# Performance work log

Measured on AMD Instinct MI355X. Metric: run time of the kernel, lower is better.

Reference implementation:

```python
import jax, jax.numpy as jnp
import numpy as np

D_CHAR, D_HID, LEN_VOC = 256, 1024, 512
BSZ, MAX_LEN = 128, 256


def setup_inputs() -> dict:
    key = jax.random.key(0)
    ks = jax.random.split(key, 14)
    s = 1.0 / np.sqrt(D_HID)  # PyTorch RNN/Linear init scale
    u = lambda k, shape: jax.random.uniform(k, shape, jnp.float32, -s, s)
    return {
        "inputs": jax.random.randint(ks[0], (BSZ, MAX_LEN), 0, LEN_VOC),
        "outputs": jax.random.randint(ks[1], (BSZ, MAX_LEN), 0, LEN_VOC),
        "emb": jax.random.normal(ks[2], (LEN_VOC, D_CHAR), jnp.float32),
        "enc_Wih": u(ks[3], (D_HID, D_CHAR)),
        "enc_Whh": u(ks[4], (D_HID, D_HID)),
        "enc_bih": u(ks[5], (D_HID,)),
        "enc_bhh": u(ks[6], (D_HID,)),
        "dec_Wih": u(ks[7], (D_HID, D_CHAR)),
        "dec_Whh": u(ks[8], (D_HID, D_HID)),
        "dec_bih": u(ks[9], (D_HID,)),
        "dec_bhh": u(ks[10], (D_HID,)),
        "out_W": u(ks[11], (LEN_VOC, D_HID)),
        "out_b": u(ks[12], (LEN_VOC,)),
    }


def rnn_scan(x_seq, h0, Wih, Whh, bih, bhh):
    """Elman RNN (tanh), batch_first input [B, T, D] -> (h_T [B,H], all h [T,B,H]).
    h_t = tanh(W_ih x_t + b_ih + W_hh h_{t-1} + b_hh), matching torch.nn.RNN."""
    # Precompute input projection for all timesteps (one big GEMM).
    xp = jnp.einsum('btd,hd->bth', x_seq, Wih) + bih + bhh  # [B,T,H]
    xp = jnp.swapaxes(xp, 0, 1)  # [T,B,H] for scan

    def step(h, x):
        h = jnp.tanh(x + h @ Whh.T)
        return h, h

    hT, hs = jax.lax.scan(step, h0, xp)
    return hT, hs


def reference(inputs, outputs, emb, enc_Wih, enc_Whh, enc_bih, enc_bhh,
              dec_Wih, dec_Whh, dec_bih, dec_bhh, out_W, out_b):
    bsz, max_len = inputs.shape
    # Encoder over input char embeddings, zero initial hidden.
    embs = emb[inputs]  # [B,T,Dc]
    h0 = jnp.zeros((bsz, D_HID), jnp.float32)
    hT, _ = rnn_scan(embs, h0, enc_Wih, enc_Whh, enc_bih, enc_bhh)
    # Teacher-forced decoder: step 0 gets zero input, step t gets emb(outputs[:, t-1]).
    dec_in = jnp.concatenate(
        [jnp.zeros((bsz, 1, D_CHAR), jnp.float32), emb[outputs[:, :-1]]], axis=1)
    _, dec_hs = rnn_scan(dec_in, hT, dec_Wih, dec_Whh, dec_bih, dec_bhh)  # [T,B,H]
    # decoder_states.transpose(0,1).view(-1, d_hid)
    states = jnp.swapaxes(dec_hs, 0, 1).reshape(-1, D_HID)  # [B*T, H]
    logits = states @ out_W.T + out_b  # [B*T, V]
    return jax.nn.log_softmax(logits, axis=1)
```

## Files before the change

kernel.cpp:

```cpp
#include <hip/hip_runtime.h>


typedef short short8 __attribute__((ext_vector_type(8)));
typedef float floatx4 __attribute__((ext_vector_type(4)));

#define WS_XP_ENC  0ull
#define WS_XP_DEC  (64ull << 20)
#define WS_STATES  (128ull << 20)
#define WS_H       (192ull << 20)
#define WS_FLAGS   ((192ull << 20) + (512ull << 10))
#define WS_WB5     (193ull << 20)
#define WS_HENC    (192ull << 20)
#define WS_FLAGS2  (256ull << 20)
#define WS_WB6     ((256ull << 20) + (1ull << 20))
#define FAST_NEED  ((265ull) << 20)

#define HS_STRIDE 1032

__device__ __forceinline__ float bf2f(unsigned short u) {
  union { unsigned u; float f; } x; x.u = ((unsigned)u) << 16; return x.f;
}
__device__ __forceinline__ unsigned short f2bf(float f) {
  union { float f; unsigned u; } x; x.f = f;
  unsigned r = x.u + 0x7FFFu + ((x.u >> 16) & 1u);
  return (unsigned short)(r >> 16);
}
__device__ __forceinline__ unsigned pkminu16(unsigned a, unsigned b) {
  unsigned d;
  asm("v_pk_min_u16 %0, %1, %2" : "=v"(d) : "v"(a), "v"(b));
  return d;
}

__global__ __launch_bounds__(256) void cvt_kernel(
    const float* __restrict__ src, unsigned short* __restrict__ dst, int n)
{
  const int i = (blockIdx.x * 256 + threadIdx.x) * 4;
  if (i >= n) return;
  const float4 v = *(const float4*)(src + i);
  unsigned short o[4] = {f2bf(v.x), f2bf(v.y), f2bf(v.z), f2bf(v.w)};
  *(uint2*)(dst + i) = *(const uint2*)o;
}

__global__ __launch_bounds__(256) void gemm_bt_kernel(
    const unsigned short* __restrict__ Abase,
    const int* __restrict__ gidx, const int mode,
    const unsigned short* __restrict__ Bmat,
    const float* __restrict__ bias0,
    const float* __restrict__ bias1,
    unsigned short* __restrict__ outp_bf,
    float* __restrict__ outp_f,
    const int K, const int N, const int nbn)
{
  __shared__ unsigned short As[64][264];
  __shared__ unsigned short Bs[64][264];
  __shared__ const unsigned short* rowsrc[64];

  const int tid = threadIdx.x;
  const int lane = tid & 63;
  const int wave = tid >> 6;
  const int bn = blockIdx.x % nbn;
  const int bm = blockIdx.x / nbn;
  const int m0 = bm * 64;
  const int j0 = bn * 64;

  if (tid < 64) {
    const int m = m0 + tid;
    const unsigned short* src;
    if (mode == 0) {
      src = Abase + (size_t)m * K;
    } else if (mode == 3) {
      src = Abase + ((size_t)(m & 255) * 128 + (m >> 8)) * 1024;
    } else {
      const int t = m >> 7;
      const int b = m & 127;
      if (mode == 2 && t == 0) {
        src = nullptr;
      } else {
        const int v = (mode == 1) ? gidx[b * 256 + t] : gidx[b * 256 + t - 1];
        src = Abase + (size_t)v * 256;
      }
    }
    rowsrc[tid] = src;
  }

  const floatx4 zf = {0.f, 0.f, 0.f, 0.f};
  floatx4 acc0 = zf, acc1 = zf, acc2 = zf, acc3 = zf;

  for (int kc = 0; kc < K; kc += 256) {
    __syncthreads();
#pragma unroll
    for (int i = 0; i < 8; ++i) {
      const int idx = i * 256 + tid;
      const int r = idx >> 5;
      const int c = idx & 31;
      const unsigned short* s = rowsrc[r];
      short8 av = {0, 0, 0, 0, 0, 0, 0, 0};
      if (s) av = *(const short8*)(s + kc + c * 8);
      *(short8*)&As[r][c * 8] = av;
      *(short8*)&Bs[r][c * 8] =
          *(const short8*)(Bmat + (size_t)(j0 + r) * K + kc + c * 8);
    }
    __syncthreads();
    const int ar = 16 * wave + (lane & 15);
    const int kq = (lane >> 4) * 8;
#pragma unroll
    for (int kk = 0; kk < 8; ++kk) {
      const short8 a = *(const short8*)&As[ar][kk * 32 + kq];
      const short8 bv0 = *(const short8*)&Bs[(lane & 15)][kk * 32 + kq];
      acc0 = __builtin_amdgcn_mfma_f32_16x16x32_bf16(a, bv0, acc0, 0, 0, 0);
      const short8 bv1 = *(const short8*)&Bs[16 + (lane & 15)][kk * 32 + kq];
      acc1 = __builtin_amdgcn_mfma_f32_16x16x32_bf16(a, bv1, acc1, 0, 0, 0);
      const short8 bv2 = *(const short8*)&Bs[32 + (lane & 15)][kk * 32 + kq];
      acc2 = __builtin_amdgcn_mfma_f32_16x16x32_bf16(a, bv2, acc2, 0, 0, 0);
      const short8 bv3 = *(const short8*)&Bs[48 + (lane & 15)][kk * 32 + kq];
      acc3 = __builtin_amdgcn_mfma_f32_16x16x32_bf16(a, bv3, acc3, 0, 0, 0);
    }
  }

  float bs[4] = {0.f, 0.f, 0.f, 0.f};
  if (bias0) {
#pragma unroll
    for (int nt = 0; nt < 4; ++nt) {
      const int jj = j0 + nt * 16 + (lane & 15);
      bs[nt] = bias0[jj] + bias1[jj];
    }
  }
  __syncthreads();
  const int rbase = 16 * wave + (lane >> 4) * 4;
  const int cl = lane & 15;

  if (outp_bf) {
#pragma unroll
    for (int i = 0; i < 4; ++i) {
      As[rbase + i][cl]      = f2bf(acc0[i] + bs[0]);
      As[rbase + i][16 + cl] = f2bf(acc1[i] + bs[1]);
      As[rbase + i][32 + cl] = f2bf(acc2[i] + bs[2]);
      As[rbase + i][48 + cl] = f2bf(acc3[i] + bs[3]);
    }
    __syncthreads();
#pragma unroll
    for (int i = 0; i < 2; ++i) {
      const int idx = i * 256 + tid;
      const int r = idx >> 3;
      const int c = idx & 7;
      *(short8*)(outp_bf + (size_t)(m0 + r) * N + j0 + c * 8) =
          *(const short8*)&As[r][c * 8];
    }
  } else {
    float (*Asf)[66] = (float(*)[66]) & As[0][0];
#pragma unroll
    for (int i = 0; i < 4; ++i) {
      Asf[rbase + i][cl]      = acc0[i] + bs[0];
      Asf[rbase + i][16 + cl] = acc1[i] + bs[1];
      Asf[rbase + i][32 + cl] = acc2[i] + bs[2];
      Asf[rbase + i][48 + cl] = acc3[i] + bs[3];
    }
    __syncthreads();
#pragma unroll
    for (int i = 0; i < 4; ++i) {
      const int idx = i * 256 + tid;
      const int r = idx >> 4;
      const int c = idx & 15;
      *(float4*)(outp_f + (size_t)(m0 + r) * N + j0 + c * 4) =
          *(const float4*)&Asf[r][c * 4];
    }
  }
}

__global__ __launch_bounds__(256) void rnn_scan2_kernel(
    const unsigned short* __restrict__ WhhE,
    const unsigned short* __restrict__ WhhD,
    const unsigned short* __restrict__ xpE,
    const unsigned short* __restrict__ xpD,
    unsigned short* __restrict__ henc,
    unsigned short* __restrict__ hdec,
    unsigned int* __restrict__ flags)
{
  __shared__ unsigned short hs[16 * HS_STRIDE];
  __shared__ unsigned int okw[4];

  const int tid = threadIdx.x;
  const int lane = tid & 63;
  const int wave = tid >> 6;
  const int g = blockIdx.x & 7;
  const int slot = blockIdx.x >> 3;
  const int b0 = g * 16;
  const int q = lane >> 4;
  const int cl = lane & 15;
  const int j = slot * 64 + wave * 16 + cl;
  unsigned int* grpflags = flags + g * 32;

  short8 w[32];
  const floatx4 zf = {0.f, 0.f, 0.f, 0.f};

  for (int phase = 0; phase < 2; ++phase) {
    const unsigned short* Whh = phase ? WhhD : WhhE;
    const unsigned short* xp = phase ? xpD : xpE;
    {
      const unsigned short* wp = Whh + (size_t)j * 1024 + q * 8;
#pragma unroll
      for (int kk = 0; kk < 32; ++kk) w[kk] = *(const short8*)(wp + kk * 32);
    }
    for (int t = 0; t < 256; ++t) {
      const int s = phase * 256 + t;
      float xpv[4];
      const unsigned short* xprow = xp + (size_t)t * 131072;
#pragma unroll
      for (int i = 0; i < 4; ++i)
        xpv[i] = bf2f(xprow[(size_t)(b0 + q * 4 + i) * 1024 + j]);

      short8 tmp[8];
      const unsigned short* hprev =
          (s <= 256 ? henc + (size_t)(s - 1) * 131072
                    : hdec + (size_t)(s - 257) * 131072) + b0 * 1024;
      if (s > 0) {
#pragma unroll
        for (int c = 0; c < 8; ++c) {
          const int gg = c * 256 + tid;
          tmp[c] = *(const short8*)(hprev + gg * 8);
        }
        const unsigned* du = (const unsigned*)tmp;
        unsigned m0v = 0xFFFFFFFFu, m1v = 0xFFFFFFFFu;
        unsigned m2v = 0xFFFFFFFFu, m3v = 0xFFFFFFFFu;
#pragma unroll
        for (int i = 0; i < 8; ++i) {
          m0v = pkminu16(m0v, du[4 * i + 0] ^ 0xAAAAAAAAu);
          m1v = pkminu16(m1v, du[4 * i + 1] ^ 0xAAAAAAAAu);
          m2v = pkminu16(m2v, du[4 * i + 2] ^ 0xAAAAAAAAu);
          m3v = pkminu16(m3v, du[4 * i + 3] ^ 0xAAAAAAAAu);
        }
        const unsigned mm = pkminu16(pkminu16(m0v, m1v), pkminu16(m2v, m3v));
        const unsigned hz = (mm - 0x00010001u) & ~mm & 0x80008000u;
        const unsigned long long bad = __ballot(hz != 0u);
        if (lane == 0) okw[wave] = (bad != 0ull) ? 1u : 0u;
      } else {
        if (lane == 0) okw[wave] = 0u;
      }
      __syncthreads();
      const bool need_fb = (okw[0] | okw[1] | okw[2] | okw[3]) != 0u;
      if (s > 0 && need_fb) {
        if (wave == 0) {
          const unsigned target = (unsigned)s;
          for (;;) {
            const unsigned f = __hip_atomic_load(&grpflags[lane & 15],
                                                 __ATOMIC_RELAXED,
                                                 __HIP_MEMORY_SCOPE_AGENT);
            if (__ballot(f < target) == 0ull) break;
            __builtin_amdgcn_s_sleep(1);
          }
        }
        __syncthreads();
#pragma unroll
        for (int c = 0; c < 8; ++c) {
          const int gg = c * 256 + tid;
          const unsigned long long* p =
              (const unsigned long long*)(hprev + gg * 8);
          union { unsigned long long u[2]; short8 s8; } v;
          v.u[0] = __hip_atomic_load(p, __ATOMIC_RELAXED,
                                     __HIP_MEMORY_SCOPE_AGENT);
          v.u[1] = __hip_atomic_load(p + 1, __ATOMIC_RELAXED,
                                     __HIP_MEMORY_SCOPE_AGENT);
          tmp[c] = v.s8;
        }
      }
      if (s > 0) {
#pragma unroll
        for (int c = 0; c < 8; ++c) {
          const int gg = c * 256 + tid;
          *(short8*)&hs[(gg >> 7) * HS_STRIDE + (gg & 127) * 8] = tmp[c];
        }
      }
      __syncthreads();

      floatx4 acc0 = zf, acc1 = zf, acc2 = zf, acc3 = zf;
      if (s > 0) {
        const unsigned short* hrow = &hs[cl * HS_STRIDE + q * 8];
#pragma unroll
        for (int kk = 0; kk < 32; kk += 4) {
          const short8 a0 = *(const short8*)(hrow + (kk + 0) * 32);
          const short8 a1 = *(const short8*)(hrow + (kk + 1) * 32);
          const short8 a2 = *(const short8*)(hrow + (kk + 2) * 32);
          const short8 a3 = *(const short8*)(hrow + (kk + 3) * 32);
          acc0 = __builtin_amdgcn_mfma_f32_16x16x32_bf16(a0, w[kk], acc0, 0, 0, 0);
          acc1 = __builtin_amdgcn_mfma_f32_16x16x32_bf16(a1, w[kk + 1], acc1, 0, 0, 0);
          acc2 = __builtin_amdgcn_mfma_f32_16x16x32_bf16(a2, w[kk + 2], acc2, 0, 0, 0);
          acc3 = __builtin_amdgcn_mfma_f32_16x16x32_bf16(a3, w[kk + 3], acc3, 0, 0, 0);
        }
      }
      unsigned short* hw =
          phase ? hdec + (size_t)t * 131072 : henc + (size_t)s * 131072;
#pragma unroll
      for (int i = 0; i < 4; ++i) {
        const int br = b0 + q * 4 + i;
        const float pre = acc0[i] + acc1[i] + acc2[i] + acc3[i] + xpv[i];
        const float e = __expf(2.f * pre);
        const float hv = 1.f - 2.f / (e + 1.f);
        const unsigned short hb = f2bf(hv);
        __hip_atomic_store(&hw[(size_t)br * 1024 + j], hb, __ATOMIC_RELAXED,
                           __HIP_MEMORY_SCOPE_AGENT);
      }
      __syncthreads();
      if (tid == 0)
        __hip_atomic_store(&grpflags[slot], (unsigned)(s + 1), __ATOMIC_RELAXED,
                           __HIP_MEMORY_SCOPE_AGENT);
    }
  }
}

__global__ __launch_bounds__(256) void rnn_scan_kernel(
    const unsigned short* __restrict__ WhhE,
    const unsigned short* __restrict__ WhhD,
    const unsigned short* __restrict__ xpE,
    const unsigned short* __restrict__ xpD,
    unsigned short* __restrict__ hbuf,
    unsigned short* __restrict__ states,
    unsigned int* __restrict__ flags)
{
  __shared__ unsigned short hs[16 * HS_STRIDE];

  const int tid = threadIdx.x;
  const int lane = tid & 63;
  const int wave = tid >> 6;
  const int g = blockIdx.x & 7;
  const int slot = blockIdx.x >> 3;
  const int b0 = g * 16;
  const int q = lane >> 4;
  const int cl = lane & 15;
  const int j = slot * 64 + wave * 16 + cl;
  unsigned int* grpflags = flags + g * 32;

  short8 w[32];
  const floatx4 zf = {0.f, 0.f, 0.f, 0.f};

  for (int phase = 0; phase < 2; ++phase) {
    const unsigned short* Whh = phase ? WhhD : WhhE;
    const unsigned short* xp = phase ? xpD : xpE;
    {
      const unsigned short* wp = Whh + (size_t)j * 1024 + q * 8;
#pragma unroll
      for (int kk = 0; kk < 32; ++kk) w[kk] = *(const short8*)(wp + kk * 32);
    }
    for (int t = 0; t < 256; ++t) {
      const int s = phase * 256 + t;
      float xpv[4];
      const unsigned short* xprow = xp + (size_t)t * 131072;
#pragma unroll
      for (int i = 0; i < 4; ++i)
        xpv[i] = bf2f(xprow[(size_t)(b0 + q * 4 + i) * 1024 + j]);

      if (s > 0) {
        const unsigned short* hrb = hbuf + (size_t)(s & 1) * 131072 + b0 * 1024;
        unsigned long long tmp[16];
#pragma unroll
        for (int c = 0; c < 8; ++c) {
          const int gg = c * 256 + tid;
          const unsigned long long* p = (const unsigned long long*)(hrb + gg * 8);
          tmp[2 * c]     = __hip_atomic_load(p, __ATOMIC_RELAXED,
                                             __HIP_MEMORY_SCOPE_AGENT);
          tmp[2 * c + 1] = __hip_atomic_load(p + 1, __ATOMIC_RELAXED,
                                             __HIP_MEMORY_SCOPE_AGENT);
        }
#pragma unroll
        for (int c = 0; c < 8; ++c) {
          const int gg = c * 256 + tid;
          unsigned long long* d =
              (unsigned long long*)&hs[(gg >> 7) * HS_STRIDE + (gg & 127) * 8];
          d[0] = tmp[2 * c];
          d[1] = tmp[2 * c + 1];
        }
      }
      __syncthreads();

      floatx4 acc0 = zf, acc1 = zf, acc2 = zf, acc3 = zf;
      if (s > 0) {
        const unsigned short* hrow = &hs[cl * HS_STRIDE + q * 8];
#pragma unroll
        for (int kk = 0; kk < 32; kk += 4) {
          const short8 a0 = *(const short8*)(hrow + (kk + 0) * 32);
          const short8 a1 = *(const short8*)(hrow + (kk + 1) * 32);
          const short8 a2 = *(const short8*)(hrow + (kk + 2) * 32);
          const short8 a3 = *(const short8*)(hrow + (kk + 3) * 32);
          acc0 = __builtin_amdgcn_mfma_f32_16x16x32_bf16(a0, w[kk], acc0, 0, 0, 0);
          acc1 = __builtin_amdgcn_mfma_f32_16x16x32_bf16(a1, w[kk + 1], acc1, 0, 0, 0);
          acc2 = __builtin_amdgcn_mfma_f32_16x16x32_bf16(a2, w[kk + 2], acc2, 0, 0, 0);
          acc3 = __builtin_amdgcn_mfma_f32_16x16x32_bf16(a3, w[kk + 3], acc3, 0, 0, 0);
        }
      }
      unsigned short* hw = hbuf + (size_t)((s + 1) & 1) * 131072;
#pragma unroll
      for (int i = 0; i < 4; ++i) {
        const int br = b0 + q * 4 + i;
        const float pre = acc0[i] + acc1[i] + acc2[i] + acc3[i] + xpv[i];
        const float e = __expf(2.f * pre);
        const float hv = 1.f - 2.f / (e + 1.f);
        const unsigned short hb = f2bf(hv);
        __hip_atomic_store(&hw[(size_t)br * 1024 + j], hb, __ATOMIC_RELAXED,
                           __HIP_MEMORY_SCOPE_AGENT);
        if (phase) states[((size_t)br * 256 + t) * 1024 + j] = hb;
      }
      __syncthreads();
      if (tid == 0)
        __hip_atomic_store(&grpflags[slot], (unsigned)(s + 1), __ATOMIC_RELAXED,
                           __HIP_MEMORY_SCOPE_AGENT);
      if (wave == 0) {
        const unsigned target = (unsigned)(s + 1);
        while (true) {
          const unsigned f = __hip_atomic_load(&grpflags[lane & 15],
                                               __ATOMIC_RELAXED,
                                               __HIP_MEMORY_SCOPE_AGENT);
          if (__ballot(f < target) == 0ull) break;
          __builtin_amdgcn_s_sleep(2);
        }
      }
      __syncthreads();
    }
  }
}

__global__ __launch_bounds__(256) void logsoftmax_kernel(
    float* __restrict__ logits, const float* __restrict__ outb)
{
  const int row = blockIdx.x * 4 + (threadIdx.x >> 6);
  const int lane = threadIdx.x & 63;
  float* rp = logits + (size_t)row * 512 + lane * 8;
  const float4 a0 = *(const float4*)rp;
  const float4 a1 = *(const float4*)(rp + 4);
  const float4 b0 = *(const float4*)(outb + lane * 8);
  const float4 b1 = *(const float4*)(outb + lane * 8 + 4);
  float v[8] = {a0.x + b0.x, a0.y + b0.y, a0.z + b0.z, a0.w + b0.w,
                a1.x + b1.x, a1.y + b1.y, a1.z + b1.z, a1.w + b1.w};
  float mx = v[0];
#pragma unroll
  for (int i = 1; i < 8; ++i) mx = fmaxf(mx, v[i]);
#pragma unroll
  for (int m = 1; m < 64; m <<= 1) mx = fmaxf(mx, __shfl_xor(mx, m, 64));
  float sum = 0.f;
#pragma unroll
  for (int i = 0; i < 8; ++i) sum += __expf(v[i] - mx);
#pragma unroll
  for (int m = 1; m < 64; m <<= 1) sum += __shfl_xor(sum, m, 64);
  const float lse = mx + __logf(sum);
  float4 o0 = {v[0] - lse, v[1] - lse, v[2] - lse, v[3] - lse};
  float4 o1 = {v[4] - lse, v[5] - lse, v[6] - lse, v[7] - lse};
  *(float4*)rp = o0;
  *(float4*)(rp + 4) = o1;
}

extern "C" void kernel_launch(void* const* d_in, const int* in_sizes, int n_in,
                              void* d_out, int out_size, void* d_ws, size_t ws_size,
                              hipStream_t stream)
{
  const int* inputs  = (const int*)d_in[0];
  const int* outputs = (const int*)d_in[1];
  const float* emb    = (const float*)d_in[2];
  const float* encWih = (const float*)d_in[3];
  const float* encWhh = (const float*)d_in[4];
  const float* encBih = (const float*)d_in[5];
  const float* encBhh = (const float*)d_in[6];
  const float* decWih = (const float*)d_in[7];
  const float* decWhh = (const float*)d_in[8];
  const float* decBih = (const float*)d_in[9];
  const float* decBhh = (const float*)d_in[10];
  const float* outW   = (const float*)d_in[11];
  const float* outB   = (const float*)d_in[12];

  char* ws = (char*)d_ws;
  unsigned short* xpE    = (unsigned short*)(ws + WS_XP_ENC);
  unsigned short* xpD    = (unsigned short*)(ws + WS_XP_DEC);
  unsigned short* states = (unsigned short*)(ws + WS_STATES);
  float* logits = (float*)d_out;

  const bool fast = (ws_size >= (size_t)FAST_NEED);
  char* wb = ws + (fast ? WS_WB6 : WS_WB5);
  unsigned short* embB  = (unsigned short*)(wb + 0);
  unsigned short* eWihB = (unsigned short*)(wb + (512ull << 10));
  unsigned short* dWihB = (unsigned short*)(wb + (1ull << 20));
  unsigned short* eWhhB = (unsigned short*)(wb + (2ull << 20));
  unsigned short* dWhhB = (unsigned short*)(wb + (4ull << 20));
  unsigned short* outWB = (unsigned short*)(wb + (6ull << 20));

  cvt_kernel<<<128, 256, 0, stream>>>(emb, embB, 512 * 256);
  cvt_kernel<<<256, 256, 0, stream>>>(encWih, eWihB, 1024 * 256);
  cvt_kernel<<<256, 256, 0, stream>>>(decWih, dWihB, 1024 * 256);
  cvt_kernel<<<1024, 256, 0, stream>>>(encWhh, eWhhB, 1024 * 1024);
  cvt_kernel<<<1024, 256, 0, stream>>>(decWhh, dWhhB, 1024 * 1024);
  cvt_kernel<<<512, 256, 0, stream>>>(outW, outWB, 512 * 1024);

  gemm_bt_kernel<<<8192, 256, 0, stream>>>(embB, inputs, 1, eWihB, encBih, encBhh,
                                           xpE, nullptr, 256, 1024, 16);
  gemm_bt_kernel<<<8192, 256, 0, stream>>>(embB, outputs, 2, dWihB, decBih, decBhh,
                                           xpD, nullptr, 256, 1024, 16);

  if (fast) {
    unsigned short* henc = (unsigned short*)(ws + WS_HENC);
    unsigned short* hdec = states;
    unsigned int* flags2 = (unsigned int*)(ws + WS_FLAGS2);
    hipMemsetAsync(flags2, 0, 4096, stream);
    rnn_scan2_kernel<<<128, 256, 0, stream>>>(eWhhB, dWhhB, xpE, xpD,
                                              henc, hdec, flags2);
    gemm_bt_kernel<<<4096, 256, 0, stream>>>(hdec, nullptr, 3, outWB, nullptr,
                                             nullptr, nullptr, logits, 1024, 512, 8);
  } else {
    unsigned short* hbuf = (unsigned short*)(ws + WS_H);
    unsigned int* flags = (unsigned int*)(ws + WS_FLAGS);
    hipMemsetAsync(flags, 0, 4096, stream);
    rnn_scan_kernel<<<128, 256, 0, stream>>>(eWhhB, dWhhB, xpE, xpD, hbuf,
                                             states, flags);
    gemm_bt_kernel<<<4096, 256, 0, stream>>>(states, nullptr, 0, outWB, nullptr,
                                             nullptr, nullptr, logits, 1024, 512, 8);
  }
  logsoftmax_kernel<<<8192, 256, 0, stream>>>(logits, outB);
}
```

Before: 1.726 ms.

## Project vocabulary once and gather input projections by token inside scan

```diff
diff --git a/kernel.cpp b/kernel.cpp
--- a/kernel.cpp
+++ b/kernel.cpp
@@ -4,16 +4,9 @@
 typedef short short8 __attribute__((ext_vector_type(8)));
 typedef float floatx4 __attribute__((ext_vector_type(4)));
 
-#define WS_XP_ENC  0ull
-#define WS_XP_DEC  (64ull << 20)
-#define WS_STATES  (128ull << 20)
-#define WS_H       (192ull << 20)
-#define WS_FLAGS   ((192ull << 20) + (512ull << 10))
-#define WS_WB5     (193ull << 20)
-#define WS_HENC    (192ull << 20)
-#define WS_FLAGS2  (256ull << 20)
-#define WS_WB6     ((256ull << 20) + (1ull << 20))
-#define FAST_NEED  ((265ull) << 20)
+#define WS_HENC   0ull
+#define WS_HDEC   (64ull << 20)
+#define WS_WB     (128ull << 20)
 
 #define HS_STRIDE 1032
 
@@ -43,7 +36,7 @@
 
 __global__ __launch_bounds__(256) void gemm_bt_kernel(
     const unsigned short* __restrict__ Abase,
-    const int* __restrict__ gidx, const int mode,
+    const int mode,
     const unsigned short* __restrict__ Bmat,
     const float* __restrict__ bias0,
     const float* __restrict__ bias1,
@@ -68,17 +61,8 @@
     const unsigned short* src;
     if (mode == 0) {
       src = Abase + (size_t)m * K;
-    } else if (mode == 3) {
+    } else {
       src = Abase + ((size_t)(m & 255) * 128 + (m >> 8)) * 1024;
-    } else {
-      const int t = m >> 7;
-      const int b = m & 127;
-      if (mode == 2 && t == 0) {
-        src = nullptr;
-      } else {
-        const int v = (mode == 1) ? gidx[b * 256 + t] : gidx[b * 256 + t - 1];
-        src = Abase + (size_t)v * 256;
-      }
     }
     rowsrc[tid] = src;
   }
@@ -94,9 +78,7 @@
       const int r = idx >> 5;
       const int c = idx & 31;
       const unsigned short* s = rowsrc[r];
-      short8 av = {0, 0, 0, 0, 0, 0, 0, 0};
-      if (s) av = *(const short8*)(s + kc + c * 8);
-      *(short8*)&As[r][c * 8] = av;
+      *(short8*)&As[r][c * 8] = *(const short8*)(s + kc + c * 8);
       *(short8*)&Bs[r][c * 8] =
           *(const short8*)(Bmat + (size_t)(j0 + r) * K + kc + c * 8);
     }
@@ -167,16 +149,21 @@
   }
 }
 
-__global__ __launch_bounds__(256) void rnn_scan2_kernel(
+__global__ __launch_bounds__(256) void rnn_scan3_kernel(
     const unsigned short* __restrict__ WhhE,
     const unsigned short* __restrict__ WhhD,
-    const unsigned short* __restrict__ xpE,
-    const unsigned short* __restrict__ xpD,
+    const unsigned short* __restrict__ projE,
+    const unsigned short* __restrict__ projD,
+    const float* __restrict__ decBih,
+    const float* __restrict__ decBhh,
+    const int* __restrict__ intoks,
+    const int* __restrict__ outtoks,
     unsigned short* __restrict__ henc,
     unsigned short* __restrict__ hdec,
     unsigned int* __restrict__ flags)
 {
   __shared__ unsigned short hs[16 * HS_STRIDE];
+  __shared__ int toks[16 * 257];
   __shared__ unsigned int okw[4];
 
   const int tid = threadIdx.x;
@@ -187,7 +174,8 @@
   const int b0 = g * 16;
   const int q = lane >> 4;
   const int cl = lane & 15;
-  const int j = slot * 64 + wave * 16 + cl;
+  const int jwb = slot * 64 + wave * 16;
+  const int jq4 = jwb + q * 4;
   unsigned int* grpflags = flags + g * 32;
 
   short8 w[32];
@@ -195,19 +183,42 @@
 
   for (int phase = 0; phase < 2; ++phase) {
     const unsigned short* Whh = phase ? WhhD : WhhE;
-    const unsigned short* xp = phase ? xpD : xpE;
+    const unsigned short* proj = phase ? projD : projE;
+    const int* gt = phase ? outtoks : intoks;
     {
-      const unsigned short* wp = Whh + (size_t)j * 1024 + q * 8;
+      const unsigned short* wp = Whh + (size_t)(jwb + cl) * 1024 + q * 8;
 #pragma unroll
       for (int kk = 0; kk < 32; ++kk) w[kk] = *(const short8*)(wp + kk * 32);
     }
+    float xb[4] = {0.f, 0.f, 0.f, 0.f};
+    if (phase) {
+#pragma unroll
+      for (int i = 0; i < 4; ++i) xb[i] = decBih[jq4 + i] + decBhh[jq4 + i];
+    }
+    __syncthreads();
+#pragma unroll
+    for (int i = 0; i < 16; ++i) {
+      const int idx = i * 256 + tid;
+      toks[(idx >> 8) * 257 + (idx & 255)] =
+          gt[(size_t)(b0 + (idx >> 8)) * 256 + (idx & 255)];
+    }
+    __syncthreads();
+
     for (int t = 0; t < 256; ++t) {
       const int s = phase * 256 + t;
-      float xpv[4];
-      const unsigned short* xprow = xp + (size_t)t * 131072;
-#pragma unroll
-      for (int i = 0; i < 4; ++i)
-        xpv[i] = bf2f(xprow[(size_t)(b0 + q * 4 + i) * 1024 + j]);
+      float xpf[4];
+      {
+        const int tt = phase ? (t > 0 ? t - 1 : 0) : t;
+        const int tok = toks[cl * 257 + tt];
+        const uint2 xr = *(const uint2*)(proj + (size_t)tok * 1024 + jq4);
+        const unsigned short* xs = (const unsigned short*)&xr;
+#pragma unroll
+        for (int i = 0; i < 4; ++i) xpf[i] = bf2f(xs[i]);
+        if (phase && t == 0) {
+#pragma unroll
+          for (int i = 0; i < 4; ++i) xpf[i] = xb[i];
+        }
+      }
 
       short8 tmp[8];
       const unsigned short* hprev =
@@ -215,10 +226,8 @@
                     : hdec + (size_t)(s - 257) * 131072) + b0 * 1024;
       if (s > 0) {
 #pragma unroll
-        for (int c = 0; c < 8; ++c) {
-          const int gg = c * 256 + tid;
-          tmp[c] = *(const short8*)(hprev + gg * 8);
-        }
+        for (int c = 0; c < 8; ++c)
+          tmp[c] = *(const short8*)(hprev + (c * 256 + tid) * 8);
         const unsigned* du = (const unsigned*)tmp;
         unsigned m0v = 0xFFFFFFFFu, m1v = 0xFFFFFFFFu;
         unsigned m2v = 0xFFFFFFFFu, m3v = 0xFFFFFFFFu;
@@ -252,9 +261,8 @@
         __syncthreads();
 #pragma unroll
         for (int c = 0; c < 8; ++c) {
-          const int gg = c * 256 + tid;
           const unsigned long long* p =
-              (const unsigned long long*)(hprev + gg * 8);
+              (const unsigned long long*)(hprev + (c * 256 + tid) * 8);
           union { unsigned long long u[2]; short8 s8; } v;
           v.u[0] = __hip_atomic_load(p, __ATOMIC_RELAXED,
                                      __HIP_MEMORY_SCOPE_AGENT);
@@ -281,138 +289,29 @@
           const short8 a1 = *(const short8*)(hrow + (kk + 1) * 32);
           const short8 a2 = *(const short8*)(hrow + (kk + 2) * 32);
           const short8 a3 = *(const short8*)(hrow + (kk + 3) * 32);
-          acc0 = __builtin_amdgcn_mfma_f32_16x16x32_bf16(a0, w[kk], acc0, 0, 0, 0);
-          acc1 = __builtin_amdgcn_mfma_f32_16x16x32_bf16(a1, w[kk + 1], acc1, 0, 0, 0);
-          acc2 = __builtin_amdgcn_mfma_f32_16x16x32_bf16(a2, w[kk + 2], acc2, 0, 0, 0);
-          acc3 = __builtin_amdgcn_mfma_f32_16x16x32_bf16(a3, w[kk + 3], acc3, 0, 0, 0);
+          acc0 = __builtin_amdgcn_mfma_f32_16x16x32_bf16(w[kk + 0], a0, acc0, 0, 0, 0);
+          acc1 = __builtin_amdgcn_mfma_f32_16x16x32_bf16(w[kk + 1], a1, acc1, 0, 0, 0);
+          acc2 = __builtin_amdgcn_mfma_f32_16x16x32_bf16(w[kk + 2], a2, acc2, 0, 0, 0);
+          acc3 = __builtin_amdgcn_mfma_f32_16x16x32_bf16(w[kk + 3], a3, acc3, 0, 0, 0);
         }
       }
       unsigned short* hw =
           phase ? hdec + (size_t)t * 131072 : henc + (size_t)s * 131072;
+      unsigned short ob[4];
 #pragma unroll
       for (int i = 0; i < 4; ++i) {
-        const int br = b0 + q * 4 + i;
-        const float pre = acc0[i] + acc1[i] + acc2[i] + acc3[i] + xpv[i];
+        const float pre = acc0[i] + acc1[i] + acc2[i] + acc3[i] + xpf[i];
         const float e = __expf(2.f * pre);
-        const float hv = 1.f - 2.f / (e + 1.f);
-        const unsigned short hb = f2bf(hv);
-        __hip_atomic_store(&hw[(size_t)br * 1024 + j], hb, __ATOMIC_RELAXED,
-                           __HIP_MEMORY_SCOPE_AGENT);
-      }
+        ob[i] = f2bf(1.f - 2.f / (e + 1.f));
+      }
+      __hip_atomic_store(
+          (unsigned long long*)(hw + (size_t)(b0 + cl) * 1024 + jq4),
+          *(const unsigned long long*)ob, __ATOMIC_RELAXED,
+          __HIP_MEMORY_SCOPE_AGENT);
       __syncthreads();
       if (tid == 0)
         __hip_atomic_store(&grpflags[slot], (unsigned)(s + 1), __ATOMIC_RELAXED,
                            __HIP_MEMORY_SCOPE_AGENT);
-    }
-  }
-}
-
-__global__ __launch_bounds__(256) void rnn_scan_kernel(
-    const unsigned short* __restrict__ WhhE,
-    const unsigned short* __restrict__ WhhD,
-    const unsigned short* __restrict__ xpE,
-    const unsigned short* __restrict__ xpD,
-    unsigned short* __restrict__ hbuf,
-    unsigned short* __restrict__ states,
-    unsigned int* __restrict__ flags)
-{
-  __shared__ unsigned short hs[16 * HS_STRIDE];
-
-  const int tid = threadIdx.x;
-  const int lane = tid & 63;
-  const int wave = tid >> 6;
-  const int g = blockIdx.x & 7;
-  const int slot = blockIdx.x >> 3;
-  const int b0 = g * 16;
-  const int q = lane >> 4;
-  const int cl = lane & 15;
-  const int j = slot * 64 + wave * 16 + cl;
-  unsigned int* grpflags = flags + g * 32;
-
-  short8 w[32];
-  const floatx4 zf = {0.f, 0.f, 0.f, 0.f};
-
-  for (int phase = 0; phase < 2; ++phase) {
-    const unsigned short* Whh = phase ? WhhD : WhhE;
-    const unsigned short* xp = phase ? xpD : xpE;
-    {
-      const unsigned short* wp = Whh + (size_t)j * 1024 + q * 8;
-#pragma unroll
-      for (int kk = 0; kk < 32; ++kk) w[kk] = *(const short8*)(wp + kk * 32);
-    }
-    for (int t = 0; t < 256; ++t) {
-      const int s = phase * 256 + t;
-      float xpv[4];
-      const unsigned short* xprow = xp + (size_t)t * 131072;
-#pragma unroll
-      for (int i = 0; i < 4; ++i)
-        xpv[i] = bf2f(xprow[(size_t)(b0 + q * 4 + i) * 1024 + j]);
-
-      if (s > 0) {
-        const unsigned short* hrb = hbuf + (size_t)(s & 1) * 131072 + b0 * 1024;
-        unsigned long long tmp[16];
-#pragma unroll
-        for (int c = 0; c < 8; ++c) {
-          const int gg = c * 256 + tid;
-          const unsigned long long* p = (const unsigned long long*)(hrb + gg * 8);
-          tmp[2 * c]     = __hip_atomic_load(p, __ATOMIC_RELAXED,
-                                             __HIP_MEMORY_SCOPE_AGENT);
-          tmp[2 * c + 1] = __hip_atomic_load(p + 1, __ATOMIC_RELAXED,
-                                             __HIP_MEMORY_SCOPE_AGENT);
-        }
-#pragma unroll
-        for (int c = 0; c < 8; ++c) {
-          const int gg = c * 256 + tid;
-          unsigned long long* d =
-              (unsigned long long*)&hs[(gg >> 7) * HS_STRIDE + (gg & 127) * 8];
-          d[0] = tmp[2 * c];
-          d[1] = tmp[2 * c + 1];
-        }
-      }
-      __syncthreads();
-
-      floatx4 acc0 = zf, acc1 = zf, acc2 = zf, acc3 = zf;
-      if (s > 0) {
-        const unsigned short* hrow = &hs[cl * HS_STRIDE + q * 8];
-#pragma unroll
-        for (int kk = 0; kk < 32; kk += 4) {
-          const short8 a0 = *(const short8*)(hrow + (kk + 0) * 32);
-          const short8 a1 = *(const short8*)(hrow + (kk + 1) * 32);
-          const short8 a2 = *(const short8*)(hrow + (kk + 2) * 32);
-          const short8 a3 = *(const short8*)(hrow + (kk + 3) * 32);
-          acc0 = __builtin_amdgcn_mfma_f32_16x16x32_bf16(a0, w[kk], acc0, 0, 0, 0);
-          acc1 = __builtin_amdgcn_mfma_f32_16x16x32_bf16(a1, w[kk + 1], acc1, 0, 0, 0);
-          acc2 = __builtin_amdgcn_mfma_f32_16x16x32_bf16(a2, w[kk + 2], acc2, 0, 0, 0);
-          acc3 = __builtin_amdgcn_mfma_f32_16x16x32_bf16(a3, w[kk + 3], acc3, 0, 0, 0);
-        }
-      }
-      unsigned short* hw = hbuf + (size_t)((s + 1) & 1) * 131072;
-#pragma unroll
-      for (int i = 0; i < 4; ++i) {
-        const int br = b0 + q * 4 + i;
-        const float pre = acc0[i] + acc1[i] + acc2[i] + acc3[i] + xpv[i];
-        const float e = __expf(2.f * pre);
-        const float hv = 1.f - 2.f / (e + 1.f);
-        const unsigned short hb = f2bf(hv);
-        __hip_atomic_store(&hw[(size_t)br * 1024 + j], hb, __ATOMIC_RELAXED,
-                           __HIP_MEMORY_SCOPE_AGENT);
-        if (phase) states[((size_t)br * 256 + t) * 1024 + j] = hb;
-      }
-      __syncthreads();
-      if (tid == 0)
-        __hip_atomic_store(&grpflags[slot], (unsigned)(s + 1), __ATOMIC_RELAXED,
-                           __HIP_MEMORY_SCOPE_AGENT);
-      if (wave == 0) {
-        const unsigned target = (unsigned)(s + 1);
-        while (true) {
-          const unsigned f = __hip_atomic_load(&grpflags[lane & 15],
-                                               __ATOMIC_RELAXED,
-                                               __HIP_MEMORY_SCOPE_AGENT);
-          if (__ballot(f < target) == 0ull) break;
-          __builtin_amdgcn_s_sleep(2);
-        }
-      }
-      __syncthreads();
     }
   }
 }
@@ -465,19 +364,21 @@
   const float* outB   = (const float*)d_in[12];
 
   char* ws = (char*)d_ws;
-  unsigned short* xpE    = (unsigned short*)(ws + WS_XP_ENC);
-  unsigned short* xpD    = (unsigned short*)(ws + WS_XP_DEC);
-  unsigned short* states = (unsigned short*)(ws + WS_STATES);
-  float* logits = (float*)d_out;
-
-  const bool fast = (ws_size >= (size_t)FAST_NEED);
-  char* wb = ws + (fast ? WS_WB6 : WS_WB5);
+  unsigned short* henc = (unsigned short*)(ws + WS_HENC);
+  unsigned short* hdec = (unsigned short*)(ws + WS_HDEC);
+  char* wb = ws + WS_WB;
   unsigned short* embB  = (unsigned short*)(wb + 0);
   unsigned short* eWihB = (unsigned short*)(wb + (512ull << 10));
   unsigned short* dWihB = (unsigned short*)(wb + (1ull << 20));
   unsigned short* eWhhB = (unsigned short*)(wb + (2ull << 20));
   unsigned short* dWhhB = (unsigned short*)(wb + (4ull << 20));
   unsigned short* outWB = (unsigned short*)(wb + (6ull << 20));
+  unsigned short* projE = (unsigned short*)(wb + (7ull << 20));
+  unsigned short* projD = (unsigned short*)(wb + (8ull << 20));
+  unsigned int*   flags = (unsigned int*)  (wb + (9ull << 20));
+  float* logits = (float*)d_out;
+
+  hipMemsetAsync(flags, 0, 4096, stream);
 
   cvt_kernel<<<128, 256, 0, stream>>>(emb, embB, 512 * 256);
   cvt_kernel<<<256, 256, 0, stream>>>(encWih, eWihB, 1024 * 256);
@@ -486,28 +387,16 @@
   cvt_kernel<<<1024, 256, 0, stream>>>(decWhh, dWhhB, 1024 * 1024);
   cvt_kernel<<<512, 256, 0, stream>>>(outW, outWB, 512 * 1024);
 
-  gemm_bt_kernel<<<8192, 256, 0, stream>>>(embB, inputs, 1, eWihB, encBih, encBhh,
-                                           xpE, nullptr, 256, 1024, 16);
-  gemm_bt_kernel<<<8192, 256, 0, stream>>>(embB, outputs, 2, dWihB, decBih, decBhh,
-                                           xpD, nullptr, 256, 1024, 16);
-
-  if (fast) {
-    unsigned short* henc = (unsigned short*)(ws + WS_HENC);
-    unsigned short* hdec = states;
-    unsigned int* flags2 = (unsigned int*)(ws + WS_FLAGS2);
-    hipMemsetAsync(flags2, 0, 4096, stream);
-    rnn_scan2_kernel<<<128, 256, 0, stream>>>(eWhhB, dWhhB, xpE, xpD,
-                                              henc, hdec, flags2);
-    gemm_bt_kernel<<<4096, 256, 0, stream>>>(hdec, nullptr, 3, outWB, nullptr,
-                                             nullptr, nullptr, logits, 1024, 512, 8);
-  } else {
-    unsigned short* hbuf = (unsigned short*)(ws + WS_H);
-    unsigned int* flags = (unsigned int*)(ws + WS_FLAGS);
-    hipMemsetAsync(flags, 0, 4096, stream);
-    rnn_scan_kernel<<<128, 256, 0, stream>>>(eWhhB, dWhhB, xpE, xpD, hbuf,
-                                             states, flags);
-    gemm_bt_kernel<<<4096, 256, 0, stream>>>(states, nullptr, 0, outWB, nullptr,
-                                             nullptr, nullptr, logits, 1024, 512, 8);
-  }
+  gemm_bt_kernel<<<128, 256, 0, stream>>>(embB, 0, eWihB, encBih, encBhh,
+                                          projE, nullptr, 256, 1024, 16);
+  gemm_bt_kernel<<<128, 256, 0, stream>>>(embB, 0, dWihB, decBih, decBhh,
+                                          projD, nullptr, 256, 1024, 16);
+
+  rnn_scan3_kernel<<<128, 256, 0, stream>>>(eWhhB, dWhhB, projE, projD,
+                                            decBih, decBhh, inputs, outputs,
+                                            henc, hdec, flags);
+
+  gemm_bt_kernel<<<4096, 256, 0, stream>>>(hdec, 3, outWB, nullptr, nullptr,
+                                           nullptr, logits, 1024, 512, 8);
   logsoftmax_kernel<<<8192, 256, 0, stream>>>(logits, outB);
 }
```

Measured after the change: 2.188 ms. 26.8% more time.
